# Performance work log

Hardware: AMD Instinct MI355X
Metric: run time of the kernel (lower is better)

## Reference

```python
import jax, jax.numpy as jnp
import numpy as np

TEMPERATURE = 0.1
BATCH = 4096
DIM = 256


def setup_inputs() -> dict:
    key = jax.random.key(0)
    k1, k2 = jax.random.split(key)
    z_i = jax.random.normal(k1, (BATCH, DIM), dtype=jnp.float32)
    z_j = jax.random.normal(k2, (BATCH, DIM), dtype=jnp.float32)
    return {"z_i": z_i, "z_j": z_j}


def reference(z_i, z_j):
    n = z_i.shape[0]
    two_n = 2 * n
    # concat both views, L2-normalize each row
    reps = jnp.concatenate([z_i, z_j], axis=0)  # [2N, D]
    reps = reps / jnp.linalg.norm(reps, axis=1, keepdims=True)
    sim = jnp.matmul(reps, reps.T) / TEMPERATURE  # [2N, 2N]
    idx = jnp.arange(two_n)
    # positive for row i is its other view: column (i + N) mod 2N
    pos = sim[idx, (idx + n) % two_n]  # [2N]
    # after removing the diagonal, logits = [positive | negatives];
    # CE with label 0  ==  -pos + logsumexp(all off-diagonal sims of the row)
    neg_inf = jnp.finfo(sim.dtype).min
    sim_masked = jnp.where(idx[:, None] == idx[None, :], neg_inf, sim)
    lse = jax.nn.logsumexp(sim_masked, axis=1)  # [2N]
    return jnp.mean(lse - pos)
```

## Files before the change

### kernel.cpp

```cpp
#include <hip/hip_runtime.h>

#define TWO_N 8192
#define HALF_N 4096
#define DIM 256
#define PANEL8 4096

#define NBLK 64
#define ROWS_PER_BLOCK 128
#define CH_COLS 64
#define CHUNK8 (CH_COLS * DIM)

#define KAPPA 14.426950408889634f
#define SQRT_KAPPA 3.7982825697f
#define LN2 0.6931471805599453f

typedef __attribute__((ext_vector_type(4))) float f32x4;
typedef __attribute__((ext_vector_type(8))) int i32x8;

__device__ __forceinline__ void async_copy16(void* lds_dst, const void* g_src) {
  __builtin_amdgcn_global_load_lds(
      (const __attribute__((address_space(1))) unsigned int*)g_src,
      (__attribute__((address_space(3))) unsigned int*)lds_dst, 16, 0, 0);
}


__device__ __forceinline__ i32x8 ld_frag(const char* p) {
  int4 lo = *reinterpret_cast<const int4*>(p);
  int4 hi = *reinterpret_cast<const int4*>(p + 1024);
  i32x8 r;
  r[0] = lo.x; r[1] = lo.y; r[2] = lo.z; r[3] = lo.w;
  r[4] = hi.x; r[5] = hi.y; r[6] = hi.z; r[7] = hi.w;
  return r;
}

__global__ __launch_bounds__(256) void k_norm(const float* __restrict__ zi,
                                              const float* __restrict__ zj,
                                              unsigned char* __restrict__ rn8,
                                              float* __restrict__ rowsum,
                                              float* __restrict__ out) {
  int p = blockIdx.x;
  int wave = threadIdx.x >> 6, lane = threadIdx.x & 63;
  int rp = wave * 4 + (lane >> 4);
  int row = p * 16 + rp;
  int kslot = lane & 15;
  int k0 = kslot * 16;
  if (threadIdx.x < 16) rowsum[p * 16 + threadIdx.x] = 0.0f;
  if (p == 0 && threadIdx.x == 0) out[0] = 0.0f;

  const float* src = (row < HALF_N) ? (zi + (size_t)row * DIM)
                                    : (zj + (size_t)(row - HALF_N) * DIM);
  float4 v0 = *reinterpret_cast<const float4*>(src + k0);
  float4 v1 = *reinterpret_cast<const float4*>(src + k0 + 4);
  float4 v2 = *reinterpret_cast<const float4*>(src + k0 + 8);
  float4 v3 = *reinterpret_cast<const float4*>(src + k0 + 12);
  float ss = v0.x*v0.x + v0.y*v0.y + v0.z*v0.z + v0.w*v0.w
           + v1.x*v1.x + v1.y*v1.y + v1.z*v1.z + v1.w*v1.w
           + v2.x*v2.x + v2.y*v2.y + v2.z*v2.z + v2.w*v2.w
           + v3.x*v3.x + v3.y*v3.y + v3.z*v3.z + v3.w*v3.w;
  #pragma unroll
  for (int m = 1; m <= 8; m <<= 1) ss += __shfl_xor(ss, m, 64);
  float r = rsqrtf(ss) * SQRT_KAPPA;

  int wA = __builtin_amdgcn_cvt_pk_fp8_f32(v0.x * r, v0.y * r, 0, 0);
  wA     = __builtin_amdgcn_cvt_pk_fp8_f32(v0.z * r, v0.w * r, wA, 1);
  int wB = __builtin_amdgcn_cvt_pk_fp8_f32(v1.x * r, v1.y * r, 0, 0);
  wB     = __builtin_amdgcn_cvt_pk_fp8_f32(v1.z * r, v1.w * r, wB, 1);
  int wC = __builtin_amdgcn_cvt_pk_fp8_f32(v2.x * r, v2.y * r, 0, 0);
  wC     = __builtin_amdgcn_cvt_pk_fp8_f32(v2.z * r, v2.w * r, wC, 1);
  int wD = __builtin_amdgcn_cvt_pk_fp8_f32(v3.x * r, v3.y * r, 0, 0);
  wD     = __builtin_amdgcn_cvt_pk_fp8_f32(v3.z * r, v3.w * r, wD, 1);

  int kh = kslot >> 3, g = (kslot >> 1) & 3, piece = kslot & 1;
  char* pb = (char*)rn8 + (size_t)p * PANEL8 + kh * 2048 + piece * 1024 +
             (g * 16 + rp) * 16;
  *reinterpret_cast<int4*>(pb) = make_int4(wA, wB, wC, wD);
}

__global__ __launch_bounds__(256, 4) void k_sim(const unsigned char* __restrict__ rn8,
                                                float* __restrict__ rowsum) {
  __shared__ alignas(16) char lds[3][CHUNK8];
  int bi = blockIdx.x;
  int s = blockIdx.y;
  if (s == 8 && bi >= 32) return;
  const int NT = (s == 8) ? 2 : 8;
  int dd0 = s * 4;
  bool sdiag = (s == 0);

  int wave = threadIdx.x >> 6, lane = threadIdx.x & 63;
  int lrow = lane & 15, kgrp = lane >> 4;
  int r0 = bi * ROWS_PER_BLOCK + wave * 32;
  const char* base = (const char*)rn8;

  i32x8 a[2][2];
  #pragma unroll
  for (int st = 0; st < 2; ++st) {
    const char* pa = base + (size_t)(bi * 8 + wave * 2 + st) * PANEL8 + lane * 16;
    #pragma unroll
    for (int kh = 0; kh < 2; ++kh)
      a[st][kh] = ld_frag(pa + kh * 2048);
  }

  float se[2][4];
  #pragma unroll
  for (int st = 0; st < 2; ++st)
    #pragma unroll
    for (int g = 0; g < 4; ++g) se[st][g] = 0.0f;

  auto stage = [&](int buf, int ch) {
    int bj = (bi + dd0 + (ch >> 1)) & (NBLK - 1);
    const char* gp = base + ((size_t)bj * 8 + (size_t)(ch & 1) * 4) * PANEL8 +
                     wave * 4096 + lane * 16;
    char* dst = &lds[buf][wave * 4096];
    async_copy16(dst, gp);
    async_copy16(dst + 1024, gp + 1024);
    async_copy16(dst + 2048, gp + 2048);
    async_copy16(dst + 3072, gp + 3072);
  };

  stage(0, 0);
  stage(1, 1);
  asm volatile("s_waitcnt vmcnt(4)" ::: "memory");
  __builtin_amdgcn_s_barrier();

  for (int ch = 0; ch < NT; ++ch) {
    if (ch + 2 < NT) stage((ch + 2) % 3, ch + 2);
    const char* lb = lds[ch % 3] + lane * 16;
    int bjc = (bi + dd0 + (ch >> 1)) & (NBLK - 1);
    bool dtile = sdiag && ((ch >> 1) == 0);
    #pragma unroll
    for (int h = 0; h < 4; ++h) {
      int colb = (ch & 1) * 64 + h * 16;
      bool d0 = dtile && (colb == wave * 32);
      bool d1 = dtile && (colb == wave * 32 + 16);
      i32x8 b0 = ld_frag(lb + h * 4096);
      i32x8 b1 = ld_frag(lb + h * 4096 + 2048);
      f32x4 acc0 = {0.f, 0.f, 0.f, 0.f};
      f32x4 acc1 = {0.f, 0.f, 0.f, 0.f};
      __builtin_amdgcn_s_setprio(1);
      acc0 = __builtin_amdgcn_mfma_scale_f32_16x16x128_f8f6f4(
                 a[0][0], b0, acc0, 0, 0, 0, 127, 0, 127);
      acc0 = __builtin_amdgcn_mfma_scale_f32_16x16x128_f8f6f4(
                 a[0][1], b1, acc0, 0, 0, 0, 127, 0, 127);
      acc1 = __builtin_amdgcn_mfma_scale_f32_16x16x128_f8f6f4(
                 a[1][0], b0, acc1, 0, 0, 0, 127, 0, 127);
      acc1 = __builtin_amdgcn_mfma_scale_f32_16x16x128_f8f6f4(
                 a[1][1], b1, acc1, 0, 0, 0, 127, 0, 127);
      __builtin_amdgcn_s_setprio(0);
      float scc = 0.0f;
      #pragma unroll
      for (int g = 0; g < 4; ++g) {
        float e0 = __builtin_amdgcn_exp2f(acc0[g]);
        float e1 = __builtin_amdgcn_exp2f(acc1[g]);
        if (d0 && lrow == kgrp * 4 + g) e0 = 0.0f;
        if (d1 && lrow == kgrp * 4 + g) e1 = 0.0f;
        se[0][g] += e0;
        se[1][g] += e1;
        scc += e0 + e1;
      }
      if (!dtile) {
        scc += __shfl_xor(scc, 16, 64);
        scc += __shfl_xor(scc, 32, 64);
        if (lane < 16)
          atomicAdd(&rowsum[bjc * ROWS_PER_BLOCK + colb + lane], scc);
      }
    }
    if (ch + 1 < NT) {
      if (ch + 2 < NT) {
        if (sdiag && ch < 2)
          asm volatile("s_waitcnt vmcnt(4)" ::: "memory");
        else
          asm volatile("s_waitcnt vmcnt(12)" ::: "memory");
      } else {
        if (NT == 2)
          asm volatile("s_waitcnt vmcnt(4)" ::: "memory");
        else
          asm volatile("s_waitcnt vmcnt(8)" ::: "memory");
      }
      __builtin_amdgcn_s_barrier();
    }
  }

  #pragma unroll
  for (int st = 0; st < 2; ++st) {
    #pragma unroll
    for (int g = 0; g < 4; ++g) {
      float v = se[st][g];
      #pragma unroll
      for (int m = 1; m <= 8; m <<= 1) v += __shfl_xor(v, m, 64);
      if (lrow == 0) atomicAdd(&rowsum[r0 + 16 * st + kgrp * 4 + g], v);
    }
  }
}

__global__ __launch_bounds__(256) void k_rowred(const unsigned char* __restrict__ rn8,
                                               const float* __restrict__ rowsum,
                                               float* __restrict__ out) {
  __shared__ float ls[4];
  int wave = threadIdx.x >> 6, lane = threadIdx.x & 63;
  int q = lane & 31;
  const char* base = (const char*)rn8;
  float local = 0.0f;
  #pragma unroll
  for (int t = 0; t < 8; ++t) {
    int i = blockIdx.x * 32 + wave * 8 + t;
    int row = (lane >> 5) ? i + HALF_N : i;
    int sl = q >> 1, jo = (q & 1) * 8;
    const char* addr = base + (size_t)(row >> 4) * PANEL8 + (sl >> 3) * 2048 +
                       ((sl >> 2) & 1) * 1024 + ((sl & 3) * 16 + (row & 15)) * 16 + jo;
    int2 own = *reinterpret_cast<const int2*>(addr);
    int px = __shfl_xor(own.x, 32, 64);
    int py = __shfl_xor(own.y, 32, 64);
    float dp =
        __builtin_amdgcn_cvt_f32_fp8(own.x, 0) * __builtin_amdgcn_cvt_f32_fp8(px, 0) +
        __builtin_amdgcn_cvt_f32_fp8(own.x, 1) * __builtin_amdgcn_cvt_f32_fp8(px, 1) +
        __builtin_amdgcn_cvt_f32_fp8(own.x, 2) * __builtin_amdgcn_cvt_f32_fp8(px, 2) +
        __builtin_amdgcn_cvt_f32_fp8(own.x, 3) * __builtin_amdgcn_cvt_f32_fp8(px, 3) +
        __builtin_amdgcn_cvt_f32_fp8(own.y, 0) * __builtin_amdgcn_cvt_f32_fp8(py, 0) +
        __builtin_amdgcn_cvt_f32_fp8(own.y, 1) * __builtin_amdgcn_cvt_f32_fp8(py, 1) +
        __builtin_amdgcn_cvt_f32_fp8(own.y, 2) * __builtin_amdgcn_cvt_f32_fp8(py, 2) +
        __builtin_amdgcn_cvt_f32_fp8(own.y, 3) * __builtin_amdgcn_cvt_f32_fp8(py, 3);
    #pragma unroll
    for (int m = 1; m <= 16; m <<= 1) dp += __shfl_xor(dp, m, 64);
    if (q == 0) {
      float lse = 10.0f + LN2 * (__builtin_amdgcn_logf(rowsum[row]) - KAPPA);
      local += lse - LN2 * dp;
    }
  }
  local += __shfl_xor(local, 32, 64);
  if (lane == 0) ls[wave] = local;
  __syncthreads();
  if (threadIdx.x == 0)
    atomicAdd(out, (ls[0] + ls[1] + ls[2] + ls[3]) * (1.0f / TWO_N));
}

extern "C" void kernel_launch(void* const* d_in, const int* in_sizes, int n_in,
                              void* d_out, int out_size, void* d_ws, size_t ws_size,
                              hipStream_t stream) {
  const float* zi = (const float*)d_in[0];
  const float* zj = (const float*)d_in[1];
  unsigned char* rn8 = (unsigned char*)d_ws;
  float* rowsum = (float*)((char*)d_ws + (size_t)TWO_N * DIM);
  float* out = (float*)d_out;

  hipLaunchKernelGGL(k_norm, dim3(TWO_N / 16), dim3(256), 0, stream,
                     zi, zj, rn8, rowsum, out);
  hipLaunchKernelGGL(k_sim, dim3(NBLK, 9), dim3(256), 0, stream, rn8, rowsum);
  hipLaunchKernelGGL(k_rowred, dim3(HALF_N / 32), dim3(256), 0, stream,
                     rn8, rowsum, out);
}
```

Before: 32.80 us.

## Quantize normalized rows to FP4 and capture positive logits inside the sim kernel

Normalized embeddings are now scaled by 16 and quantized to FP4 (e2m1) with a threshold encoder, which halves the packed panel size, the LDS staging, and the async copies per chunk. The MFMA runs in FP4 mode with a post-scale applied before exp2. The positive-pair similarities are written out from the s==8 diagonal tile of k_sim, so k_rowred no longer recomputes dot products from the quantized data. The risk is that FP4 precision loss may push the loss outside tolerance, and the FP4 MFMA may run no faster per instruction than FP8 at this size.

```diff
diff --git a/kernel.cpp b/kernel.cpp
--- a/kernel.cpp
+++ b/kernel.cpp
@@ -3,15 +3,16 @@
 #define TWO_N 8192
 #define HALF_N 4096
 #define DIM 256
-#define PANEL8 4096
+#define PANEL4 2048
 
 #define NBLK 64
 #define ROWS_PER_BLOCK 128
 #define CH_COLS 64
-#define CHUNK8 (CH_COLS * DIM)
+#define CHUNK4 (CH_COLS * DIM / 2)
 
 #define KAPPA 14.426950408889634f
-#define SQRT_KAPPA 3.7982825697f
+#define KINV  (KAPPA / 256.0f)
+#define POS_SCALE (10.0f / 256.0f)
 #define LN2 0.6931471805599453f
 
 typedef __attribute__((ext_vector_type(4))) float f32x4;
@@ -24,18 +25,24 @@
 }
 
 
-__device__ __forceinline__ i32x8 ld_frag(const char* p) {
-  int4 lo = *reinterpret_cast<const int4*>(p);
-  int4 hi = *reinterpret_cast<const int4*>(p + 1024);
+__device__ __forceinline__ unsigned int fp4e(float x) {
+  unsigned int s = (__float_as_uint(x) >> 31) << 3;
+  float a = fabsf(x);
+  unsigned int c = (a > 0.25f) + (a > 0.75f) + (a > 1.25f) + (a > 1.75f)
+                 + (a > 2.5f) + (a > 3.5f) + (a > 5.0f);
+  return s | c;
+}
+
+__device__ __forceinline__ i32x8 up8(int4 v) {
   i32x8 r;
-  r[0] = lo.x; r[1] = lo.y; r[2] = lo.z; r[3] = lo.w;
-  r[4] = hi.x; r[5] = hi.y; r[6] = hi.z; r[7] = hi.w;
+  r[0] = v.x; r[1] = v.y; r[2] = v.z; r[3] = v.w;
+  r[4] = 0; r[5] = 0; r[6] = 0; r[7] = 0;
   return r;
 }
 
 __global__ __launch_bounds__(256) void k_norm(const float* __restrict__ zi,
                                               const float* __restrict__ zj,
-                                              unsigned char* __restrict__ rn8,
+                                              unsigned char* __restrict__ rn4,
                                               float* __restrict__ rowsum,
                                               float* __restrict__ out) {
   int p = blockIdx.x;
@@ -59,45 +66,47 @@
            + v3.x*v3.x + v3.y*v3.y + v3.z*v3.z + v3.w*v3.w;
   #pragma unroll
   for (int m = 1; m <= 8; m <<= 1) ss += __shfl_xor(ss, m, 64);
-  float r = rsqrtf(ss) * SQRT_KAPPA;
-
-  int wA = __builtin_amdgcn_cvt_pk_fp8_f32(v0.x * r, v0.y * r, 0, 0);
-  wA     = __builtin_amdgcn_cvt_pk_fp8_f32(v0.z * r, v0.w * r, wA, 1);
-  int wB = __builtin_amdgcn_cvt_pk_fp8_f32(v1.x * r, v1.y * r, 0, 0);
-  wB     = __builtin_amdgcn_cvt_pk_fp8_f32(v1.z * r, v1.w * r, wB, 1);
-  int wC = __builtin_amdgcn_cvt_pk_fp8_f32(v2.x * r, v2.y * r, 0, 0);
-  wC     = __builtin_amdgcn_cvt_pk_fp8_f32(v2.z * r, v2.w * r, wC, 1);
-  int wD = __builtin_amdgcn_cvt_pk_fp8_f32(v3.x * r, v3.y * r, 0, 0);
-  wD     = __builtin_amdgcn_cvt_pk_fp8_f32(v3.z * r, v3.w * r, wD, 1);
+  float r = rsqrtf(ss) * 16.0f;
+
+  unsigned int w0 =  fp4e(v0.x * r)        | (fp4e(v0.y * r) << 4)
+                  | (fp4e(v0.z * r) << 8)  | (fp4e(v0.w * r) << 12)
+                  | (fp4e(v1.x * r) << 16) | (fp4e(v1.y * r) << 20)
+                  | (fp4e(v1.z * r) << 24) | (fp4e(v1.w * r) << 28);
+  unsigned int w1 =  fp4e(v2.x * r)        | (fp4e(v2.y * r) << 4)
+                  | (fp4e(v2.z * r) << 8)  | (fp4e(v2.w * r) << 12)
+                  | (fp4e(v3.x * r) << 16) | (fp4e(v3.y * r) << 20)
+                  | (fp4e(v3.z * r) << 24) | (fp4e(v3.w * r) << 28);
 
   int kh = kslot >> 3, g = (kslot >> 1) & 3, piece = kslot & 1;
-  char* pb = (char*)rn8 + (size_t)p * PANEL8 + kh * 2048 + piece * 1024 +
-             (g * 16 + rp) * 16;
-  *reinterpret_cast<int4*>(pb) = make_int4(wA, wB, wC, wD);
-}
-
-__global__ __launch_bounds__(256, 4) void k_sim(const unsigned char* __restrict__ rn8,
-                                                float* __restrict__ rowsum) {
-  __shared__ alignas(16) char lds[3][CHUNK8];
+  char* pb = (char*)rn4 + (size_t)p * PANEL4 + kh * 1024 +
+             (g * 16 + rp) * 16 + piece * 8;
+  *reinterpret_cast<uint2*>(pb) = make_uint2(w0, w1);
+}
+
+__global__ __launch_bounds__(256, 4) void k_sim(const unsigned char* __restrict__ rn4,
+                                                float* __restrict__ rowsum,
+                                                float* __restrict__ posv) {
+  __shared__ alignas(16) char lds[3][CHUNK4];
   int bi = blockIdx.x;
   int s = blockIdx.y;
   if (s == 8 && bi >= 32) return;
   const int NT = (s == 8) ? 2 : 8;
   int dd0 = s * 4;
   bool sdiag = (s == 0);
+  bool ptile = (s == 8);
 
   int wave = threadIdx.x >> 6, lane = threadIdx.x & 63;
   int lrow = lane & 15, kgrp = lane >> 4;
   int r0 = bi * ROWS_PER_BLOCK + wave * 32;
-  const char* base = (const char*)rn8;
-
-  i32x8 a[2][2];
+  const char* base = (const char*)rn4;
+
+  int4 a[2][2];
   #pragma unroll
   for (int st = 0; st < 2; ++st) {
-    const char* pa = base + (size_t)(bi * 8 + wave * 2 + st) * PANEL8 + lane * 16;
+    const char* pa = base + (size_t)(bi * 8 + wave * 2 + st) * PANEL4 + lane * 16;
     #pragma unroll
     for (int kh = 0; kh < 2; ++kh)
-      a[st][kh] = ld_frag(pa + kh * 2048);
+      a[st][kh] = *reinterpret_cast<const int4*>(pa + kh * 1024);
   }
 
   float se[2][4];
@@ -108,18 +117,16 @@
 
   auto stage = [&](int buf, int ch) {
     int bj = (bi + dd0 + (ch >> 1)) & (NBLK - 1);
-    const char* gp = base + ((size_t)bj * 8 + (size_t)(ch & 1) * 4) * PANEL8 +
-                     wave * 4096 + lane * 16;
-    char* dst = &lds[buf][wave * 4096];
+    const char* gp = base + ((size_t)bj * 8 + (size_t)(ch & 1) * 4 + wave) * PANEL4 +
+                     lane * 16;
+    char* dst = &lds[buf][wave * 2048];
     async_copy16(dst, gp);
     async_copy16(dst + 1024, gp + 1024);
-    async_copy16(dst + 2048, gp + 2048);
-    async_copy16(dst + 3072, gp + 3072);
   };
 
   stage(0, 0);
   stage(1, 1);
-  asm volatile("s_waitcnt vmcnt(4)" ::: "memory");
+  asm volatile("s_waitcnt vmcnt(2)" ::: "memory");
   __builtin_amdgcn_s_barrier();
 
   for (int ch = 0; ch < NT; ++ch) {
@@ -132,27 +139,33 @@
       int colb = (ch & 1) * 64 + h * 16;
       bool d0 = dtile && (colb == wave * 32);
       bool d1 = dtile && (colb == wave * 32 + 16);
-      i32x8 b0 = ld_frag(lb + h * 4096);
-      i32x8 b1 = ld_frag(lb + h * 4096 + 2048);
+      bool p0 = ptile && (colb == wave * 32);
+      bool p1 = ptile && (colb == wave * 32 + 16);
+      int4 b0 = *reinterpret_cast<const int4*>(lb + h * 2048);
+      int4 b1 = *reinterpret_cast<const int4*>(lb + h * 2048 + 1024);
       f32x4 acc0 = {0.f, 0.f, 0.f, 0.f};
       f32x4 acc1 = {0.f, 0.f, 0.f, 0.f};
       __builtin_amdgcn_s_setprio(1);
       acc0 = __builtin_amdgcn_mfma_scale_f32_16x16x128_f8f6f4(
-                 a[0][0], b0, acc0, 0, 0, 0, 127, 0, 127);
+                 up8(a[0][0]), up8(b0), acc0, 4, 4, 0, 127, 0, 127);
       acc0 = __builtin_amdgcn_mfma_scale_f32_16x16x128_f8f6f4(
-                 a[0][1], b1, acc0, 0, 0, 0, 127, 0, 127);
+                 up8(a[0][1]), up8(b1), acc0, 4, 4, 0, 127, 0, 127);
       acc1 = __builtin_amdgcn_mfma_scale_f32_16x16x128_f8f6f4(
-                 a[1][0], b0, acc1, 0, 0, 0, 127, 0, 127);
+                 up8(a[1][0]), up8(b0), acc1, 4, 4, 0, 127, 0, 127);
       acc1 = __builtin_amdgcn_mfma_scale_f32_16x16x128_f8f6f4(
-                 a[1][1], b1, acc1, 0, 0, 0, 127, 0, 127);
+                 up8(a[1][1]), up8(b1), acc1, 4, 4, 0, 127, 0, 127);
       __builtin_amdgcn_s_setprio(0);
       float scc = 0.0f;
       #pragma unroll
       for (int g = 0; g < 4; ++g) {
-        float e0 = __builtin_amdgcn_exp2f(acc0[g]);
-        float e1 = __builtin_amdgcn_exp2f(acc1[g]);
+        float e0 = __builtin_amdgcn_exp2f(acc0[g] * KINV);
+        float e1 = __builtin_amdgcn_exp2f(acc1[g] * KINV);
         if (d0 && lrow == kgrp * 4 + g) e0 = 0.0f;
         if (d1 && lrow == kgrp * 4 + g) e1 = 0.0f;
+        if (p0 && lrow == kgrp * 4 + g)
+          posv[r0 + kgrp * 4 + g] = acc0[g];
+        if (p1 && lrow == kgrp * 4 + g)
+          posv[r0 + 16 + kgrp * 4 + g] = acc1[g];
         se[0][g] += e0;
         se[1][g] += e1;
         scc += e0 + e1;
@@ -165,17 +178,12 @@
       }
     }
     if (ch + 1 < NT) {
-      if (ch + 2 < NT) {
-        if (sdiag && ch < 2)
-          asm volatile("s_waitcnt vmcnt(4)" ::: "memory");
-        else
-          asm volatile("s_waitcnt vmcnt(12)" ::: "memory");
-      } else {
-        if (NT == 2)
-          asm volatile("s_waitcnt vmcnt(4)" ::: "memory");
-        else
-          asm volatile("s_waitcnt vmcnt(8)" ::: "memory");
-      }
+      if (sdiag && ch < 2)
+        asm volatile("s_waitcnt vmcnt(2)" ::: "memory");
+      else if (NT == 2)
+        asm volatile("s_waitcnt vmcnt(4)" ::: "memory");
+      else
+        asm volatile("s_waitcnt vmcnt(6)" ::: "memory");
       __builtin_amdgcn_s_barrier();
     }
   }
@@ -192,41 +200,21 @@
   }
 }
 
-__global__ __launch_bounds__(256) void k_rowred(const unsigned char* __restrict__ rn8,
-                                               const float* __restrict__ rowsum,
+__global__ __launch_bounds__(256) void k_rowred(const float* __restrict__ rowsum,
+                                               const float* __restrict__ posv,
                                                float* __restrict__ out) {
   __shared__ float ls[4];
   int wave = threadIdx.x >> 6, lane = threadIdx.x & 63;
-  int q = lane & 31;
-  const char* base = (const char*)rn8;
   float local = 0.0f;
   #pragma unroll
-  for (int t = 0; t < 8; ++t) {
-    int i = blockIdx.x * 32 + wave * 8 + t;
-    int row = (lane >> 5) ? i + HALF_N : i;
-    int sl = q >> 1, jo = (q & 1) * 8;
-    const char* addr = base + (size_t)(row >> 4) * PANEL8 + (sl >> 3) * 2048 +
-                       ((sl >> 2) & 1) * 1024 + ((sl & 3) * 16 + (row & 15)) * 16 + jo;
-    int2 own = *reinterpret_cast<const int2*>(addr);
-    int px = __shfl_xor(own.x, 32, 64);
-    int py = __shfl_xor(own.y, 32, 64);
-    float dp =
-        __builtin_amdgcn_cvt_f32_fp8(own.x, 0) * __builtin_amdgcn_cvt_f32_fp8(px, 0) +
-        __builtin_amdgcn_cvt_f32_fp8(own.x, 1) * __builtin_amdgcn_cvt_f32_fp8(px, 1) +
-        __builtin_amdgcn_cvt_f32_fp8(own.x, 2) * __builtin_amdgcn_cvt_f32_fp8(px, 2) +
-        __builtin_amdgcn_cvt_f32_fp8(own.x, 3) * __builtin_amdgcn_cvt_f32_fp8(px, 3) +
-        __builtin_amdgcn_cvt_f32_fp8(own.y, 0) * __builtin_amdgcn_cvt_f32_fp8(py, 0) +
-        __builtin_amdgcn_cvt_f32_fp8(own.y, 1) * __builtin_amdgcn_cvt_f32_fp8(py, 1) +
-        __builtin_amdgcn_cvt_f32_fp8(own.y, 2) * __builtin_amdgcn_cvt_f32_fp8(py, 2) +
-        __builtin_amdgcn_cvt_f32_fp8(own.y, 3) * __builtin_amdgcn_cvt_f32_fp8(py, 3);
-    #pragma unroll
-    for (int m = 1; m <= 16; m <<= 1) dp += __shfl_xor(dp, m, 64);
-    if (q == 0) {
-      float lse = 10.0f + LN2 * (__builtin_amdgcn_logf(rowsum[row]) - KAPPA);
-      local += lse - LN2 * dp;
-    }
-  }
-  local += __shfl_xor(local, 32, 64);
+  for (int t = 0; t < 2; ++t) {
+    int r = blockIdx.x * 512 + t * 256 + threadIdx.x;
+    int pr = (r < HALF_N) ? r : r - HALF_N;
+    float lse = 10.0f + LN2 * (__builtin_amdgcn_logf(rowsum[r]) - KAPPA);
+    local += lse - POS_SCALE * posv[pr];
+  }
+  #pragma unroll
+  for (int m = 1; m <= 32; m <<= 1) local += __shfl_xor(local, m, 64);
   if (lane == 0) ls[wave] = local;
   __syncthreads();
   if (threadIdx.x == 0)
@@ -238,13 +226,15 @@
                               hipStream_t stream) {
   const float* zi = (const float*)d_in[0];
   const float* zj = (const float*)d_in[1];
-  unsigned char* rn8 = (unsigned char*)d_ws;
-  float* rowsum = (float*)((char*)d_ws + (size_t)TWO_N * DIM);
+  unsigned char* rn4 = (unsigned char*)d_ws;
+  float* rowsum = (float*)((char*)d_ws + (size_t)TWO_N * DIM / 2);
+  float* posv = rowsum + TWO_N;
   float* out = (float*)d_out;
 
   hipLaunchKernelGGL(k_norm, dim3(TWO_N / 16), dim3(256), 0, stream,
-                     zi, zj, rn8, rowsum, out);
-  hipLaunchKernelGGL(k_sim, dim3(NBLK, 9), dim3(256), 0, stream, rn8, rowsum);
-  hipLaunchKernelGGL(k_rowred, dim3(HALF_N / 32), dim3(256), 0, stream,
-                     rn8, rowsum, out);
-}
+                     zi, zj, rn4, rowsum, out);
+  hipLaunchKernelGGL(k_sim, dim3(NBLK, 9), dim3(256), 0, stream,
+                     rn4, rowsum, posv);
+  hipLaunchKernelGGL(k_rowred, dim3(TWO_N / 512), dim3(256), 0, stream,
+                     rowsum, posv, out);
+}
```

Result: faster. 27.60 us (median of 2 runs) (-15.8%).
